# Performance work log

Hardware: AMD Instinct MI355X
Metric: run time of the kernel (lower is better)

## Reference

```python
import jax, jax.numpy as jnp
import numpy as np

# Block-structured decompression constants (SFACTOR=2 on 32x32 channels)
RBLKS, CBLKS = 2, 2      # blocks per axis
RPIX, CPIX = 8, 8        # compressed block size
OUT_HW = 32              # decompressed channel size
B = 32768


def setup_inputs() -> dict:
    key = jax.random.key(0)
    k1, k2, k3, k4 = jax.random.split(key, 4)
    x = jax.random.normal(k1, (B, 3, 16, 16), dtype=jnp.float32)
    # per-row-block decompression matrices: [rblks, 2*RPIX, RPIX]
    lhs = jax.random.normal(k2, (RBLKS, 2 * RPIX, RPIX), dtype=jnp.float32) * 0.1
    # per-col-block decompression matrices: [cblks, CPIX, 2*CPIX]
    rhs = jax.random.normal(k3, (CBLKS, CPIX, 2 * CPIX), dtype=jnp.float32) * 0.1
    W = jax.random.normal(k4, (1, 3 * 32 * 32), dtype=jnp.float32) * 0.02
    b = jnp.zeros((1,), dtype=jnp.float32)
    return {"x": x, "lhs": lhs, "rhs": rhs, "W": W, "b": b}


def _decompress(xc, lhs, rhs):
    # xc: [B, 16, 16] compressed channel -> [B, 32, 32]
    n = xc.shape[0]
    # split into [B, rblk, RPIX, cblk, CPIX] blocks
    blocks = xc.reshape(n, RBLKS, RPIX, CBLKS, CPIX)
    # per-block: out_block = lhs[r] @ block @ rhs[c]  (block-wise bfloat16 decompression math)
    out = jnp.einsum('rPp,brpcq,cqQ->brPcQ', lhs, blocks, rhs)
    return out.reshape(n, OUT_HW, OUT_HW)


def reference(x, lhs, rhs, W, b):
    # three per-channel decompression calls, as in the original forward
    r = _decompress(x[:, 0], lhs, rhs)
    g = _decompress(x[:, 1], lhs, rhs)
    bch = _decompress(x[:, 2], lhs, rhs)
    out = jnp.stack((r, g, bch), axis=1)            # [B, 3, 32, 32]
    out = out.reshape(-1, 3 * 32 * 32)              # [B, 3072]
    return out @ W.T + b                            # [B, 1]
```

## Files before the change

kernel.cpp:

```cpp
#include <hip/hip_runtime.h>
#include <hip/hip_bf16.h>


#define BATCH 32768
#define ROW_F4 192
#define ROWS_PER_BLOCK 16
#define GRID_BLOCKS (BATCH / ROWS_PER_BLOCK)

__device__ __forceinline__ float dot4(const float4& a, const float4& b) {
    return a.x * b.x + a.y * b.y + a.z * b.z + a.w * b.w;
}

__device__ __forceinline__ void reduce4_store(float a0, float a1, float a2, float a3,
                                              int lane, float* __restrict__ outp,
                                              float bias) {
    a0 += __shfl_xor(a0, 1);
    a1 += __shfl_xor(a1, 1);
    a2 += __shfl_xor(a2, 1);
    a3 += __shfl_xor(a3, 1);
    float b0 = (lane & 1) ? a1 : a0;
    float b1 = (lane & 1) ? a3 : a2;
    b0 += __shfl_xor(b0, 2);
    b1 += __shfl_xor(b1, 2);
    float c = (lane & 2) ? b1 : b0;
    c += __shfl_xor(c, 4);
    c += __shfl_xor(c, 8);
    c += __shfl_xor(c, 16);
    c += __shfl_xor(c, 32);
    if (lane < 4) outp[lane] = c + bias;
}

__global__ __launch_bounds__(256, 4) void fused_compressor_kernel(
        const float4* __restrict__ x4,
        const float4* __restrict__ lhs4,
        const float4* __restrict__ rhs4,
        const float4* __restrict__ W4,
        const float* __restrict__ bptr,
        float* __restrict__ out) {
    __shared__ __align__(16) float Wl[3072];
    __shared__ __align__(16) float rh[256];
    __shared__ __align__(16) float lh[256];
    __shared__ float tmp[1536];
    __shared__ __align__(16) float weff[768];

    const int tid  = threadIdx.x;
    const int lane = tid & 63;
    const int w    = tid >> 6;

    const int row0 = blockIdx.x * ROWS_PER_BLOCK + w * 4;

    float4 wreg0 = W4[tid];
    float4 wreg1 = W4[tid + 256];
    float4 wreg2 = W4[tid + 512];
    int sidx = tid & 127;
    float4 sreg = (sidx < 64) ? rhs4[sidx] : lhs4[sidx - 64];
    __builtin_amdgcn_sched_barrier(0);

    const float4* xr = x4 + (size_t)row0 * ROW_F4 + lane;
    float4 xv[4][3];
    #pragma unroll
    for (int rr = 0; rr < 4; ++rr)
        #pragma unroll
        for (int k = 0; k < 3; ++k)
            xv[rr][k] = xr[rr * ROW_F4 + k * 64];
    __builtin_amdgcn_sched_barrier(0);

    reinterpret_cast<float4*>(Wl)[tid]       = wreg0;
    reinterpret_cast<float4*>(Wl)[tid + 256] = wreg1;
    reinterpret_cast<float4*>(Wl)[tid + 512] = wreg2;
    if (tid < 128) {
        if (tid < 64) reinterpret_cast<float4*>(rh)[tid] = sreg;
        else          reinterpret_cast<float4*>(lh)[tid - 64] = sreg;
    }
    __syncthreads();

    const float4* rhv = reinterpret_cast<const float4*>(rh);
    const float4* Wlv = reinterpret_cast<const float4*>(Wl);
    #pragma unroll
    for (int s = 0; s < 6; ++s) {
        int idx = tid + (s << 8);
        int ch  = idx >> 9;
        int rem = idx & 511;
        int R   = rem >> 4;
        int j   = rem & 15;
        int c   = j >> 3;
        int q   = j & 7;
        const float4* rp = rhv + c * 32 + q * 4;
        const float4* wp = Wlv + ch * 256 + R * 8 + c * 4;
        tmp[idx] = dot4(rp[0], wp[0]) + dot4(rp[1], wp[1])
                 + dot4(rp[2], wp[2]) + dot4(rp[3], wp[3]);
    }
    __syncthreads();

    #pragma unroll
    for (int s = 0; s < 3; ++s) {
        int idx = tid + (s << 8);
        int ch  = idx >> 8;
        int rem = idx & 255;
        int i   = rem >> 4;
        int j   = rem & 15;
        int r   = i >> 3;
        int p   = i & 7;
        const float* lp = lh + r * 128 + p;
        const float* tp = tmp + ch * 512 + r * 256 + j;
        float acc = 0.f;
        #pragma unroll
        for (int P = 0; P < 16; ++P) acc += lp[P * 8] * tp[P * 16];
        weff[idx] = acc;
    }
    __syncthreads();

    const float4* w4 = reinterpret_cast<const float4*>(weff);
    const float4 wv0 = w4[lane];
    const float4 wv1 = w4[lane + 64];
    const float4 wv2 = w4[lane + 128];
    const float  bias = bptr[0];

    float a0 = dot4(xv[0][0], wv0) + dot4(xv[0][1], wv1) + dot4(xv[0][2], wv2);
    float a1 = dot4(xv[1][0], wv0) + dot4(xv[1][1], wv1) + dot4(xv[1][2], wv2);
    float a2 = dot4(xv[2][0], wv0) + dot4(xv[2][1], wv1) + dot4(xv[2][2], wv2);
    float a3 = dot4(xv[3][0], wv0) + dot4(xv[3][1], wv1) + dot4(xv[3][2], wv2);
    reduce4_store(a0, a1, a2, a3, lane, out + row0, bias);
}

extern "C" void kernel_launch(void* const* d_in, const int* in_sizes, int n_in,
                              void* d_out, int out_size, void* d_ws, size_t ws_size,
                              hipStream_t stream) {
    const float* x   = (const float*)d_in[0];
    const float* lhs = (const float*)d_in[1];
    const float* rhs = (const float*)d_in[2];
    const float* W   = (const float*)d_in[3];
    const float* b   = (const float*)d_in[4];
    float* out = (float*)d_out;

    fused_compressor_kernel<<<GRID_BLOCKS, 256, 0, stream>>>(
        (const float4*)x, (const float4*)lhs, (const float4*)rhs,
        (const float4*)W, b, out);
}
```

Measured before the change: 21.69 us.

## Process 32 rows per block with double-buffered x loads across row pairs

Doubles rows per block so each wave handles 8 rows, halving how many times the per-block effective-weight precompute runs. The x rows are loaded in two register buffers of two rows each, and the next pair's loads are issued while the current pair is being reduced. The sched barriers are removed and x loads are issued before the W loads. This cuts redundant weight-folding work and keeps memory loads in flight, at the cost of fewer blocks and possibly more register pressure.

```diff
diff --git a/kernel.cpp b/kernel.cpp
--- a/kernel.cpp
+++ b/kernel.cpp
@@ -4,30 +4,25 @@
 
 #define BATCH 32768
 #define ROW_F4 192
-#define ROWS_PER_BLOCK 16
+#define ROWS_PER_BLOCK 32
 #define GRID_BLOCKS (BATCH / ROWS_PER_BLOCK)
 
 __device__ __forceinline__ float dot4(const float4& a, const float4& b) {
     return a.x * b.x + a.y * b.y + a.z * b.z + a.w * b.w;
 }
 
-__device__ __forceinline__ void reduce4_store(float a0, float a1, float a2, float a3,
-                                              int lane, float* __restrict__ outp,
+__device__ __forceinline__ void reduce2_store(float a0, float a1, int lane,
+                                              float* __restrict__ outp,
                                               float bias) {
     a0 += __shfl_xor(a0, 1);
     a1 += __shfl_xor(a1, 1);
-    a2 += __shfl_xor(a2, 1);
-    a3 += __shfl_xor(a3, 1);
-    float b0 = (lane & 1) ? a1 : a0;
-    float b1 = (lane & 1) ? a3 : a2;
-    b0 += __shfl_xor(b0, 2);
-    b1 += __shfl_xor(b1, 2);
-    float c = (lane & 2) ? b1 : b0;
-    c += __shfl_xor(c, 4);
-    c += __shfl_xor(c, 8);
-    c += __shfl_xor(c, 16);
-    c += __shfl_xor(c, 32);
-    if (lane < 4) outp[lane] = c + bias;
+    float b = (lane & 1) ? a1 : a0;
+    b += __shfl_xor(b, 2);
+    b += __shfl_xor(b, 4);
+    b += __shfl_xor(b, 8);
+    b += __shfl_xor(b, 16);
+    b += __shfl_xor(b, 32);
+    if (lane < 2) outp[lane] = b + bias;
 }
 
 __global__ __launch_bounds__(256, 4) void fused_compressor_kernel(
@@ -47,23 +42,26 @@
     const int lane = tid & 63;
     const int w    = tid >> 6;
 
-    const int row0 = blockIdx.x * ROWS_PER_BLOCK + w * 4;
+    const int wrow = blockIdx.x * ROWS_PER_BLOCK + w * 8;
+
+    const float4* xr = x4 + (size_t)wrow * ROW_F4 + lane;
+    float4 xa[2][3], xb[2][3];
+    #pragma unroll
+    for (int r = 0; r < 2; ++r)
+        #pragma unroll
+        for (int k = 0; k < 3; ++k)
+            xa[r][k] = xr[r * ROW_F4 + k * 64];
+    #pragma unroll
+    for (int r = 0; r < 2; ++r)
+        #pragma unroll
+        for (int k = 0; k < 3; ++k)
+            xb[r][k] = xr[(2 + r) * ROW_F4 + k * 64];
 
     float4 wreg0 = W4[tid];
     float4 wreg1 = W4[tid + 256];
     float4 wreg2 = W4[tid + 512];
     int sidx = tid & 127;
     float4 sreg = (sidx < 64) ? rhs4[sidx] : lhs4[sidx - 64];
-    __builtin_amdgcn_sched_barrier(0);
-
-    const float4* xr = x4 + (size_t)row0 * ROW_F4 + lane;
-    float4 xv[4][3];
-    #pragma unroll
-    for (int rr = 0; rr < 4; ++rr)
-        #pragma unroll
-        for (int k = 0; k < 3; ++k)
-            xv[rr][k] = xr[rr * ROW_F4 + k * 64];
-    __builtin_amdgcn_sched_barrier(0);
 
     reinterpret_cast<float4*>(Wl)[tid]       = wreg0;
     reinterpret_cast<float4*>(Wl)[tid + 256] = wreg1;
@@ -110,17 +108,42 @@
     }
     __syncthreads();
 
-    const float4* w4 = reinterpret_cast<const float4*>(weff);
-    const float4 wv0 = w4[lane];
-    const float4 wv1 = w4[lane + 64];
-    const float4 wv2 = w4[lane + 128];
+    const float4* wv4 = reinterpret_cast<const float4*>(weff);
+    const float4 wv0 = wv4[lane];
+    const float4 wv1 = wv4[lane + 64];
+    const float4 wv2 = wv4[lane + 128];
     const float  bias = bptr[0];
 
-    float a0 = dot4(xv[0][0], wv0) + dot4(xv[0][1], wv1) + dot4(xv[0][2], wv2);
-    float a1 = dot4(xv[1][0], wv0) + dot4(xv[1][1], wv1) + dot4(xv[1][2], wv2);
-    float a2 = dot4(xv[2][0], wv0) + dot4(xv[2][1], wv1) + dot4(xv[2][2], wv2);
-    float a3 = dot4(xv[3][0], wv0) + dot4(xv[3][1], wv1) + dot4(xv[3][2], wv2);
-    reduce4_store(a0, a1, a2, a3, lane, out + row0, bias);
+    {
+        float a0 = dot4(xa[0][0], wv0) + dot4(xa[0][1], wv1) + dot4(xa[0][2], wv2);
+        float a1 = dot4(xa[1][0], wv0) + dot4(xa[1][1], wv1) + dot4(xa[1][2], wv2);
+        #pragma unroll
+        for (int r = 0; r < 2; ++r)
+            #pragma unroll
+            for (int k = 0; k < 3; ++k)
+                xa[r][k] = xr[(4 + r) * ROW_F4 + k * 64];
+        reduce2_store(a0, a1, lane, out + wrow, bias);
+    }
+    {
+        float a0 = dot4(xb[0][0], wv0) + dot4(xb[0][1], wv1) + dot4(xb[0][2], wv2);
+        float a1 = dot4(xb[1][0], wv0) + dot4(xb[1][1], wv1) + dot4(xb[1][2], wv2);
+        #pragma unroll
+        for (int r = 0; r < 2; ++r)
+            #pragma unroll
+            for (int k = 0; k < 3; ++k)
+                xb[r][k] = xr[(6 + r) * ROW_F4 + k * 64];
+        reduce2_store(a0, a1, lane, out + wrow + 2, bias);
+    }
+    {
+        float a0 = dot4(xa[0][0], wv0) + dot4(xa[0][1], wv1) + dot4(xa[0][2], wv2);
+        float a1 = dot4(xa[1][0], wv0) + dot4(xa[1][1], wv1) + dot4(xa[1][2], wv2);
+        reduce2_store(a0, a1, lane, out + wrow + 4, bias);
+    }
+    {
+        float a0 = dot4(xb[0][0], wv0) + dot4(xb[0][1], wv1) + dot4(xb[0][2], wv2);
+        float a1 = dot4(xb[1][0], wv0) + dot4(xb[1][1], wv1) + dot4(xb[1][2], wv2);
+        reduce2_store(a0, a1, lane, out + wrow + 6, bias);
+    }
 }
 
 extern "C" void kernel_launch(void* const* d_in, const int* in_sizes, int n_in,
```

New measurement: 20.64 us. -4.9%, faster.
